# Performance work log

Hardware: AMD Instinct MI355X
Metric: run time of the kernel (lower is better)

## Reference

```python
import jax, jax.numpy as jnp
import numpy as np

SIZE = 512

def _corner_means(x):
    # x: [B, C, H, W]; top-left corner nested-shell means via integral image.
    cs = jnp.cumsum(jnp.cumsum(x, axis=2), axis=3)          # [B, C, H, W]
    d = jnp.diagonal(cs, axis1=2, axis2=3)[..., :SIZE]      # [B, C, SIZE] = sum of i x i corner window
    shell = jnp.concatenate([d[..., :1], d[..., 1:] - d[..., :-1]], axis=-1)
    counts = (2 * jnp.arange(1, SIZE + 1) - 1).astype(x.dtype)  # i*i - (i-1)*(i-1)
    return shell / counts                                    # [B, C, SIZE]

def setup_inputs() -> dict:
    key = jax.random.key(0)
    x = jax.random.normal(key, (32, 8, 512, 512), dtype=jnp.float32)
    return {"x": x}

def reference(x):
    tl = _corner_means(x)
    tr = _corner_means(x[:, :, :, ::-1])
    bl = _corner_means(x[:, :, ::-1, :])
    br = _corner_means(x[:, :, ::-1, ::-1])
    # each [B, C, SIZE] -> [B, SIZE, C]; concat corners on channel dim -> [B, SIZE, 4C]
    out = jnp.concatenate(
        [jnp.swapaxes(t, 1, 2) for t in (tl, tr, bl, br)], axis=2
    )
    return out
```

## Files before the change

kernel.cpp:

```cpp
#include <hip/hip_runtime.h>


#define PLANES 256
#define WW     512
#define HH     512
#define JBLK   16
#define RPB    32
#define WPB    4
#define PF     4

__device__ __forceinline__ float wave_sum64(float v) {
  v += __int_as_float(__builtin_amdgcn_update_dpp(0, __float_as_int(v), 0x111, 0xf, 0xf, true));
  v += __int_as_float(__builtin_amdgcn_update_dpp(0, __float_as_int(v), 0x112, 0xf, 0xf, true));
  v += __int_as_float(__builtin_amdgcn_update_dpp(0, __float_as_int(v), 0x114, 0xf, 0xf, true));
  v += __int_as_float(__builtin_amdgcn_update_dpp(0, __float_as_int(v), 0x118, 0xf, 0xf, true));
  v += __int_as_float(__builtin_amdgcn_update_dpp(0, __float_as_int(v), 0x142, 0xf, 0xf, true));
  v += __int_as_float(__builtin_amdgcn_update_dpp(0, __float_as_int(v), 0x143, 0xf, 0xf, true));
  return v;
}

__global__ __launch_bounds__(256, 4)
void corner_pass1(const float* __restrict__ x, float* __restrict__ wsA,
                  float* __restrict__ wsBT) {
  const int t     = threadIdx.x;
  const int lane  = t & 63;
  const int wv    = t >> 6;
  const int plane = blockIdx.y;
  const int jb    = blockIdx.x * WPB + wv;
  const int r0    = jb * RPB;
  const int c0    = lane << 3;

  const float4* base = (const float4*)(x + (size_t)plane * HH * WW + (size_t)r0 * WW);
  const int li = lane * 2;

  float4 b0[PF], b1[PF];
#pragma unroll
  for (int i = 0; i < PF; ++i) {
    b0[i] = base[i * 128 + li];
    b1[i] = base[i * 128 + li + 1];
  }

  float cs[8] = {0.f, 0.f, 0.f, 0.f, 0.f, 0.f, 0.f, 0.f};

#pragma unroll 4
  for (int rr = 0; rr < RPB; ++rr) {
    const int r = r0 + rr;
    const int q = 511 - r;

    const float4 va = b0[rr & (PF - 1)];
    const float4 vb = b1[rr & (PF - 1)];
    if (rr + PF < RPB) {
      b0[rr & (PF - 1)] = base[(rr + PF) * 128 + li];
      b1[rr & (PF - 1)] = base[(rr + PF) * 128 + li + 1];
    }

    cs[0] += va.x; cs[1] += va.y; cs[2] += va.z; cs[3] += va.w;
    cs[4] += vb.x; cs[5] += vb.y; cs[6] += vb.z; cs[7] += vb.w;

    const float p0 = va.x, p1 = p0 + va.y, p2 = p1 + va.z, p3 = p2 + va.w;
    const float p4 = p3 + vb.x, p5 = p4 + vb.y, p6 = p5 + vb.z, p7 = p6 + vb.w;

    const int lt1 = (r - 1) - c0;
    const int lt2 = q - c0;
    float m1 = 0.f;
    m1 = (lt1 >= 0) ? p0 : m1; m1 = (lt1 >= 1) ? p1 : m1;
    m1 = (lt1 >= 2) ? p2 : m1; m1 = (lt1 >= 3) ? p3 : m1;
    m1 = (lt1 >= 4) ? p4 : m1; m1 = (lt1 >= 5) ? p5 : m1;
    m1 = (lt1 >= 6) ? p6 : m1; m1 = (lt1 >= 7) ? p7 : m1;
    float m2 = 0.f;
    m2 = (lt2 >= 0) ? p0 : m2; m2 = (lt2 >= 1) ? p1 : m2;
    m2 = (lt2 >= 2) ? p2 : m2; m2 = (lt2 >= 3) ? p3 : m2;
    m2 = (lt2 >= 4) ? p4 : m2; m2 = (lt2 >= 5) ? p5 : m2;
    m2 = (lt2 >= 6) ? p6 : m2; m2 = (lt2 >= 7) ? p7 : m2;

    float T = p7;
    T  = wave_sum64(T);
    m1 = wave_sum64(m1);
    m2 = wave_sum64(m2);

    const int k1 = r & 7, k2 = q & 7;
    float selA = cs[0];
    selA = (k1 == 1) ? cs[1] : selA; selA = (k1 == 2) ? cs[2] : selA;
    selA = (k1 == 3) ? cs[3] : selA; selA = (k1 == 4) ? cs[4] : selA;
    selA = (k1 == 5) ? cs[5] : selA; selA = (k1 == 6) ? cs[6] : selA;
    selA = (k1 == 7) ? cs[7] : selA;
    float selB = cs[0];
    selB = (k2 == 1) ? cs[1] : selB; selB = (k2 == 2) ? cs[2] : selB;
    selB = (k2 == 3) ? cs[3] : selB; selB = (k2 == 4) ? cs[4] : selB;
    selB = (k2 == 5) ? cs[5] : selB; selB = (k2 == 7) ? cs[7] : selB;
    selB = (k2 == 6) ? cs[6] : selB;

    const float a = __shfl(selA, r >> 3, 64);
    const float b = __shfl(selB, q >> 3, 64);

    if (lane == 63) {
      float4 A;
      A.x = m1 + a;
      A.y = T - m2 + b;
      A.z = m2 - b;
      A.w = T - m1 - a;
      ((float4*)wsA)[(size_t)plane * 512 + r] = A;
    }
  }

  float4* bt = (float4*)(wsBT + ((size_t)plane * JBLK + jb) * WW + c0);
  bt[0] = make_float4(cs[0], cs[1], cs[2], cs[3]);
  bt[1] = make_float4(cs[4], cs[5], cs[6], cs[7]);
}

__global__ __launch_bounds__(256)
void corner_pass2(const float* __restrict__ wsA, const float* __restrict__ wsBT,
                  float* __restrict__ out) {
  const int idx   = blockIdx.x * 256 + threadIdx.x;
  const int plane = idx >> 9;
  const int r     = idx & 511;
  const int q     = 511 - r;

  const float4 A  = ((const float4*)wsA)[idx];
  const float* bt = wsBT + (size_t)plane * JBLK * 512;

  const int jb = r >> 5;
  float prev_r = 0.f, tot_r = 0.f, prev_q = 0.f, tot_q = 0.f;
#pragma unroll
  for (int jj = 0; jj < JBLK; ++jj) {
    const float br_ = bt[jj * 512 + r];
    const float bq_ = bt[jj * 512 + q];
    tot_r += br_; tot_q += bq_;
    if (jj < jb) { prev_r += br_; prev_q += bq_; }
  }

  const float TL = A.x + prev_r;
  const float TR = A.y + prev_q;
  const float BL = A.z + (tot_q - prev_q);
  const float BR = A.w + (tot_r - prev_r);

  const float invr = 1.0f / (float)(2 * r + 1);
  const float invq = 1.0f / (float)(2 * q + 1);

  const int b = plane >> 3, c = plane & 7;
  float* ob = out + (size_t)b * 512 * 32;
  ob[r * 32 + c]      = TL * invr;
  ob[r * 32 + 8 + c]  = TR * invr;
  ob[q * 32 + 16 + c] = BL * invq;
  ob[q * 32 + 24 + c] = BR * invq;
}

extern "C" void kernel_launch(void* const* d_in, const int* in_sizes, int n_in,
                              void* d_out, int out_size, void* d_ws, size_t ws_size,
                              hipStream_t stream) {
  const float* x = (const float*)d_in[0];
  float* out = (float*)d_out;

  float* wsA  = (float*)d_ws;
  float* wsBT = wsA + (size_t)PLANES * 512 * 4;

  dim3 g1(JBLK / WPB, PLANES);
  corner_pass1<<<g1, 256, 0, stream>>>(x, wsA, wsBT);
  corner_pass2<<<512, 256, 0, stream>>>(wsA, wsBT, out);
}
```

Before: 366.6 us.

## Fuse two passes via per-plane atomic last-block completion; static register selects

Merges the second pass into the first kernel. Each block increments a per-plane atomic counter, and the last block to finish for a plane computes the output for that plane, which removes one kernel launch. The row loop is restructured into an 8-wide inner unroll, so the column-sum index becomes a compile-time constant and the runtime select chains over cs[] go away. The cost is an extra memset launch for the counters, thread fences, and a tail phase that runs on only one block per plane.

```diff
diff --git a/kernel.cpp b/kernel.cpp
--- a/kernel.cpp
+++ b/kernel.cpp
@@ -7,6 +7,7 @@
 #define JBLK   16
 #define RPB    32
 #define WPB    4
+#define BPP    (JBLK / WPB)
 #define PF     4
 
 __device__ __forceinline__ float wave_sum64(float v) {
@@ -20,8 +21,9 @@
 }
 
 __global__ __launch_bounds__(256, 4)
-void corner_pass1(const float* __restrict__ x, float* __restrict__ wsA,
-                  float* __restrict__ wsBT) {
+void corner_fused(const float* __restrict__ x, float* __restrict__ wsA,
+                  float* __restrict__ wsBT, unsigned* __restrict__ counters,
+                  float* __restrict__ out) {
   const int t     = threadIdx.x;
   const int lane  = t & 63;
   const int wv    = t >> 6;
@@ -42,107 +44,109 @@
 
   float cs[8] = {0.f, 0.f, 0.f, 0.f, 0.f, 0.f, 0.f, 0.f};
 
-#pragma unroll 4
-  for (int rr = 0; rr < RPB; ++rr) {
-    const int r = r0 + rr;
-    const int q = 511 - r;
+  for (int rr8 = 0; rr8 < RPB; rr8 += 8) {
+#pragma unroll
+    for (int u = 0; u < 8; ++u) {
+      const int rr = rr8 + u;
+      const int r  = r0 + rr;
+      const int q  = 511 - r;
 
-    const float4 va = b0[rr & (PF - 1)];
-    const float4 vb = b1[rr & (PF - 1)];
-    if (rr + PF < RPB) {
-      b0[rr & (PF - 1)] = base[(rr + PF) * 128 + li];
-      b1[rr & (PF - 1)] = base[(rr + PF) * 128 + li + 1];
-    }
+      const float4 va = b0[rr & (PF - 1)];
+      const float4 vb = b1[rr & (PF - 1)];
+      if (rr + PF < RPB) {
+        b0[rr & (PF - 1)] = base[(rr + PF) * 128 + li];
+        b1[rr & (PF - 1)] = base[(rr + PF) * 128 + li + 1];
+      }
 
-    cs[0] += va.x; cs[1] += va.y; cs[2] += va.z; cs[3] += va.w;
-    cs[4] += vb.x; cs[5] += vb.y; cs[6] += vb.z; cs[7] += vb.w;
+      cs[0] += va.x; cs[1] += va.y; cs[2] += va.z; cs[3] += va.w;
+      cs[4] += vb.x; cs[5] += vb.y; cs[6] += vb.z; cs[7] += vb.w;
 
-    const float p0 = va.x, p1 = p0 + va.y, p2 = p1 + va.z, p3 = p2 + va.w;
-    const float p4 = p3 + vb.x, p5 = p4 + vb.y, p6 = p5 + vb.z, p7 = p6 + vb.w;
+      const float p0 = va.x, p1 = p0 + va.y, p2 = p1 + va.z, p3 = p2 + va.w;
+      const float p4 = p3 + vb.x, p5 = p4 + vb.y, p6 = p5 + vb.z, p7 = p6 + vb.w;
 
-    const int lt1 = (r - 1) - c0;
-    const int lt2 = q - c0;
-    float m1 = 0.f;
-    m1 = (lt1 >= 0) ? p0 : m1; m1 = (lt1 >= 1) ? p1 : m1;
-    m1 = (lt1 >= 2) ? p2 : m1; m1 = (lt1 >= 3) ? p3 : m1;
-    m1 = (lt1 >= 4) ? p4 : m1; m1 = (lt1 >= 5) ? p5 : m1;
-    m1 = (lt1 >= 6) ? p6 : m1; m1 = (lt1 >= 7) ? p7 : m1;
-    float m2 = 0.f;
-    m2 = (lt2 >= 0) ? p0 : m2; m2 = (lt2 >= 1) ? p1 : m2;
-    m2 = (lt2 >= 2) ? p2 : m2; m2 = (lt2 >= 3) ? p3 : m2;
-    m2 = (lt2 >= 4) ? p4 : m2; m2 = (lt2 >= 5) ? p5 : m2;
-    m2 = (lt2 >= 6) ? p6 : m2; m2 = (lt2 >= 7) ? p7 : m2;
+      const int lt1 = (r - 1) - c0;
+      const int lt2 = q - c0;
+      float m1 = 0.f;
+      m1 = (lt1 >= 0) ? p0 : m1; m1 = (lt1 >= 1) ? p1 : m1;
+      m1 = (lt1 >= 2) ? p2 : m1; m1 = (lt1 >= 3) ? p3 : m1;
+      m1 = (lt1 >= 4) ? p4 : m1; m1 = (lt1 >= 5) ? p5 : m1;
+      m1 = (lt1 >= 6) ? p6 : m1; m1 = (lt1 >= 7) ? p7 : m1;
+      float m2 = 0.f;
+      m2 = (lt2 >= 0) ? p0 : m2; m2 = (lt2 >= 1) ? p1 : m2;
+      m2 = (lt2 >= 2) ? p2 : m2; m2 = (lt2 >= 3) ? p3 : m2;
+      m2 = (lt2 >= 4) ? p4 : m2; m2 = (lt2 >= 5) ? p5 : m2;
+      m2 = (lt2 >= 6) ? p6 : m2; m2 = (lt2 >= 7) ? p7 : m2;
 
-    float T = p7;
-    T  = wave_sum64(T);
-    m1 = wave_sum64(m1);
-    m2 = wave_sum64(m2);
+      float T = p7;
+      T  = wave_sum64(T);
+      m1 = wave_sum64(m1);
+      m2 = wave_sum64(m2);
 
-    const int k1 = r & 7, k2 = q & 7;
-    float selA = cs[0];
-    selA = (k1 == 1) ? cs[1] : selA; selA = (k1 == 2) ? cs[2] : selA;
-    selA = (k1 == 3) ? cs[3] : selA; selA = (k1 == 4) ? cs[4] : selA;
-    selA = (k1 == 5) ? cs[5] : selA; selA = (k1 == 6) ? cs[6] : selA;
-    selA = (k1 == 7) ? cs[7] : selA;
-    float selB = cs[0];
-    selB = (k2 == 1) ? cs[1] : selB; selB = (k2 == 2) ? cs[2] : selB;
-    selB = (k2 == 3) ? cs[3] : selB; selB = (k2 == 4) ? cs[4] : selB;
-    selB = (k2 == 5) ? cs[5] : selB; selB = (k2 == 7) ? cs[7] : selB;
-    selB = (k2 == 6) ? cs[6] : selB;
+      const float a = __shfl(cs[u],     r >> 3, 64);
+      const float b = __shfl(cs[7 - u], q >> 3, 64);
 
-    const float a = __shfl(selA, r >> 3, 64);
-    const float b = __shfl(selB, q >> 3, 64);
-
-    if (lane == 63) {
-      float4 A;
-      A.x = m1 + a;
-      A.y = T - m2 + b;
-      A.z = m2 - b;
-      A.w = T - m1 - a;
-      ((float4*)wsA)[(size_t)plane * 512 + r] = A;
+      if (lane == 63) {
+        float4 A;
+        A.x = m1 + a;
+        A.y = T - m2 + b;
+        A.z = m2 - b;
+        A.w = T - m1 - a;
+        ((float4*)wsA)[(size_t)plane * 512 + r] = A;
+      }
     }
   }
 
-  float4* bt = (float4*)(wsBT + ((size_t)plane * JBLK + jb) * WW + c0);
-  bt[0] = make_float4(cs[0], cs[1], cs[2], cs[3]);
-  bt[1] = make_float4(cs[4], cs[5], cs[6], cs[7]);
-}
-
-__global__ __launch_bounds__(256)
-void corner_pass2(const float* __restrict__ wsA, const float* __restrict__ wsBT,
-                  float* __restrict__ out) {
-  const int idx   = blockIdx.x * 256 + threadIdx.x;
-  const int plane = idx >> 9;
-  const int r     = idx & 511;
-  const int q     = 511 - r;
-
-  const float4 A  = ((const float4*)wsA)[idx];
-  const float* bt = wsBT + (size_t)plane * JBLK * 512;
-
-  const int jb = r >> 5;
-  float prev_r = 0.f, tot_r = 0.f, prev_q = 0.f, tot_q = 0.f;
-#pragma unroll
-  for (int jj = 0; jj < JBLK; ++jj) {
-    const float br_ = bt[jj * 512 + r];
-    const float bq_ = bt[jj * 512 + q];
-    tot_r += br_; tot_q += bq_;
-    if (jj < jb) { prev_r += br_; prev_q += bq_; }
+  {
+    float4* bt = (float4*)(wsBT + ((size_t)plane * JBLK + jb) * WW + c0);
+    bt[0] = make_float4(cs[0], cs[1], cs[2], cs[3]);
+    bt[1] = make_float4(cs[4], cs[5], cs[6], cs[7]);
   }
 
-  const float TL = A.x + prev_r;
-  const float TR = A.y + prev_q;
-  const float BL = A.z + (tot_q - prev_q);
-  const float BR = A.w + (tot_r - prev_r);
+  __shared__ int sdone;
+  __syncthreads();
+  __threadfence();
+  if (t == 0) {
+    const unsigned old = atomicAdd(&counters[plane], 1u);
+    sdone = (old == BPP - 1);
+  }
+  __syncthreads();
+  if (!sdone) return;
+  __threadfence();
 
-  const float invr = 1.0f / (float)(2 * r + 1);
-  const float invq = 1.0f / (float)(2 * q + 1);
+  const float*  btp = wsBT + (size_t)plane * JBLK * WW;
+  const float4* Ap  = (const float4*)wsA + (size_t)plane * 512;
+  const int bb = plane >> 3, cc = plane & 7;
+  float* ob = out + (size_t)bb * 512 * 32;
 
-  const int b = plane >> 3, c = plane & 7;
-  float* ob = out + (size_t)b * 512 * 32;
-  ob[r * 32 + c]      = TL * invr;
-  ob[r * 32 + 8 + c]  = TR * invr;
-  ob[q * 32 + 16 + c] = BL * invq;
-  ob[q * 32 + 24 + c] = BR * invq;
+#pragma unroll
+  for (int h = 0; h < 2; ++h) {
+    const int r = t + h * 256;
+    const int q = 511 - r;
+    const float4 A = Ap[r];
+
+    const int jbr = r >> 5;
+    float prev_r = 0.f, tot_r = 0.f, prev_q = 0.f, tot_q = 0.f;
+#pragma unroll
+    for (int jj = 0; jj < JBLK; ++jj) {
+      const float br_ = btp[jj * WW + r];
+      const float bq_ = btp[jj * WW + q];
+      tot_r += br_; tot_q += bq_;
+      if (jj < jbr) { prev_r += br_; prev_q += bq_; }
+    }
+
+    const float TL = A.x + prev_r;
+    const float TR = A.y + prev_q;
+    const float BL = A.z + (tot_q - prev_q);
+    const float BR = A.w + (tot_r - prev_r);
+
+    const float invr = 1.0f / (float)(2 * r + 1);
+    const float invq = 1.0f / (float)(2 * q + 1);
+
+    ob[r * 32 + cc]      = TL * invr;
+    ob[r * 32 + 8 + cc]  = TR * invr;
+    ob[q * 32 + 16 + cc] = BL * invq;
+    ob[q * 32 + 24 + cc] = BR * invq;
+  }
 }
 
 extern "C" void kernel_launch(void* const* d_in, const int* in_sizes, int n_in,
@@ -151,10 +155,12 @@
   const float* x = (const float*)d_in[0];
   float* out = (float*)d_out;
 
-  float* wsA  = (float*)d_ws;
-  float* wsBT = wsA + (size_t)PLANES * 512 * 4;
+  float*    wsA      = (float*)d_ws;
+  float*    wsBT     = wsA + (size_t)PLANES * 512 * 4;
+  unsigned* counters = (unsigned*)(wsBT + (size_t)PLANES * JBLK * WW);
 
-  dim3 g1(JBLK / WPB, PLANES);
-  corner_pass1<<<g1, 256, 0, stream>>>(x, wsA, wsBT);
-  corner_pass2<<<512, 256, 0, stream>>>(wsA, wsBT, out);
+  hipMemsetAsync(counters, 0, PLANES * sizeof(unsigned), stream);
+
+  dim3 g1(BPP, PLANES);
+  corner_fused<<<g1, 256, 0, stream>>>(x, wsA, wsBT, counters, out);
 }
```

Result: slower. 648.7 us (+76.9%).
